# Kernel tuning notes

Measured on AMD Instinct MI355X. Metric: run time of the kernel, lower is better.

The kernel has to match this reference:

```python
import jax, jax.numpy as jnp
import numpy as np
from jax import lax


def setup_inputs() -> dict:
    key = jax.random.key(0)
    k1, k2 = jax.random.split(key)
    x = jax.random.normal(k1, (16, 224, 224, 256), dtype=jnp.float32)
    # Conv2D(1, 7): kernel HWIO [7,7,2,1], glorot-ish scale
    conv_w = jax.random.normal(k2, (7, 7, 2, 1), dtype=jnp.float32) * 0.1
    conv_b = jnp.zeros((1,), dtype=jnp.float32)
    return {"x": x, "conv_w": conv_w, "conv_b": conv_b}


def reference(x, conv_w, conv_b):
    # channel-wise stats: [B,H,W,1] each
    max_pool = jnp.max(x, axis=-1, keepdims=True)
    avg_pool = jnp.mean(x, axis=-1, keepdims=True)
    concat = jnp.concatenate([max_pool, avg_pool], axis=-1)  # [B,H,W,2]
    attn = lax.conv_general_dilated(
        concat, conv_w,
        window_strides=(1, 1), padding='SAME',
        dimension_numbers=('NHWC', 'HWIO', 'NHWC'))
    attn = jax.nn.sigmoid(attn + conv_b)  # [B,H,W,1]
    return x * attn
```

## Files before the change

kernel.cpp:

```cpp
#include <hip/hip_runtime.h>
#include <math.h>

#define B_ 16
#define H_ 224
#define W_ 224
#define C_ 256
#define IMGPIX (H_*W_)
#define NBLK 2048
#define NWAVE (NBLK*4)
#define NGRP  (NBLK*16)

typedef float f32x4 __attribute__((ext_vector_type(4)));

__device__ __forceinline__ void mul_role(const float* __restrict__ x,
                                         const float* __restrict__ cw,
                                         const float* __restrict__ cb,
                                         float* __restrict__ out,
                                         const float2* __restrict__ pooled,
                                         int mb0, int t) {
    const int lane = t & 63;
    float wm = 0.0f, wa = 0.0f;
    if (lane < 49) { wm = cw[lane * 2]; wa = cw[lane * 2 + 1]; }
    const float bias = cb[0];
    const int kh = lane / 7 - 3;
    const int kw = lane % 7 - 3;
    const int gw = blockIdx.x * 4 + (t >> 6);

    for (int q = gw; q < 2 * IMGPIX; q += NWAVE) {
        const int img = q / IMGPIX;
        const int px  = q - img * IMGPIX;
        const int b   = mb0 + img;
        const float*  xb    = x   + (size_t)b * IMGPIX * C_;
        float*        ob    = out + (size_t)b * IMGPIX * C_;
        const float2* pbase = pooled + (size_t)b * IMGPIX;

        const int h = px / W_, w = px % W_;
        float acc = 0.0f;
        if (lane < 49) {
            const int hh = h + kh, ww = w + kw;
            if (hh >= 0 && hh < H_ && ww >= 0 && ww < W_) {
                const float2 pv = pbase[hh * W_ + ww];
                acc = fmaf(pv.x, wm, pv.y * wa);
            }
        }
        #pragma unroll
        for (int off = 1; off < 64; off <<= 1) acc += __shfl_xor(acc, off);
        const float attn = 1.0f / (1.0f + expf(-(acc + bias)));

        f32x4 v = ((const f32x4*)(xb + (size_t)px * C_))[lane];
        v.x *= attn; v.y *= attn; v.z *= attn; v.w *= attn;
        __builtin_nontemporal_store(v, &((f32x4*)ob)[(size_t)px * 64 + lane]);
    }
}

__device__ __forceinline__ void pool_role(const float* __restrict__ x,
                                          float2* __restrict__ pooled,
                                          int pb0, int t) {
    const int gg  = blockIdx.x * 16 + (t >> 4);
    const int sub = t & 15;

    for (int q = gg; q < 2 * IMGPIX; q += NGRP) {
        const int img = q / IMGPIX;
        const int px  = q - img * IMGPIX;
        const int b   = pb0 + img;
        const float* xb  = x + (size_t)b * IMGPIX * C_;
        float2*      pot = pooled + (size_t)b * IMGPIX;

        const f32x4* p4 = (const f32x4*)(xb + (size_t)px * C_);
        float m = -INFINITY, s = 0.0f;
        #pragma unroll
        for (int j = 0; j < 4; ++j) {
            f32x4 v = p4[j * 16 + sub];
            m = fmaxf(m, fmaxf(fmaxf(v.x, v.y), fmaxf(v.z, v.w)));
            s += (v.x + v.y) + (v.z + v.w);
        }
        #pragma unroll
        for (int off = 1; off < 16; off <<= 1) {
            m = fmaxf(m, __shfl_xor(m, off));
            s += __shfl_xor(s, off);
        }
        if (sub == 0) pot[px] = make_float2(m, s * (1.0f / 256.0f));
    }
}

__global__ __launch_bounds__(256) void step_kernel(const float* __restrict__ x,
                                                   const float* __restrict__ cw,
                                                   const float* __restrict__ cb,
                                                   float* __restrict__ out,
                                                   float2* __restrict__ pooled,
                                                   int mb0, int pb0) {
    const int t = threadIdx.x;
    if (blockIdx.x & 1) {
        if (mb0 >= 0) mul_role(x, cw, cb, out, pooled, mb0, t);
        if (pb0 >= 0) pool_role(x, pooled, pb0, t);
    } else {
        if (pb0 >= 0) pool_role(x, pooled, pb0, t);
        if (mb0 >= 0) mul_role(x, cw, cb, out, pooled, mb0, t);
    }
}

extern "C" void kernel_launch(void* const* d_in, const int* in_sizes, int n_in,
                              void* d_out, int out_size, void* d_ws, size_t ws_size,
                              hipStream_t stream) {
    const float* x  = (const float*)d_in[0];
    const float* cw = (const float*)d_in[1];
    const float* cb = (const float*)d_in[2];
    float* out      = (float*)d_out;
    float2* pooled  = (float2*)d_ws;

    for (int d = 0; d <= 8; ++d) {
        const int mb0 = (d >= 1) ? 2 * (d - 1) : -1;
        const int pb0 = (d < 8) ? 2 * d : -1;
        step_kernel<<<NBLK, 256, 0, stream>>>(x, cw, cb, out, pooled, mb0, pb0);
    }
}
```

Baseline: 412.6 us.

## Split conv/sigmoid into separate pipeline stage writing a per-pixel attention map

The 7x7 conv and sigmoid move out of the multiply pass into their own attn_role, which writes a per-pixel attention map to workspace. The launch sequence becomes a three-stage software pipeline (pool, attn, mul) over 10 launches, with block roles rotated by blockIdx%3. The multiply pass now reads only x and one attention scalar per pixel, dropping the 49-tap gather and shuffle reduction from the bandwidth-bound loop. In exchange it adds one extra launch, an extra workspace array and its traffic, and unbalanced role ordering across blocks.

```diff
diff --git a/kernel.cpp b/kernel.cpp
--- a/kernel.cpp
+++ b/kernel.cpp
@@ -12,61 +12,16 @@
 
 typedef float f32x4 __attribute__((ext_vector_type(4)));
 
-__device__ __forceinline__ void mul_role(const float* __restrict__ x,
-                                         const float* __restrict__ cw,
-                                         const float* __restrict__ cb,
-                                         float* __restrict__ out,
-                                         const float2* __restrict__ pooled,
-                                         int mb0, int t) {
-    const int lane = t & 63;
-    float wm = 0.0f, wa = 0.0f;
-    if (lane < 49) { wm = cw[lane * 2]; wa = cw[lane * 2 + 1]; }
-    const float bias = cb[0];
-    const int kh = lane / 7 - 3;
-    const int kw = lane % 7 - 3;
-    const int gw = blockIdx.x * 4 + (t >> 6);
-
-    for (int q = gw; q < 2 * IMGPIX; q += NWAVE) {
-        const int img = q / IMGPIX;
-        const int px  = q - img * IMGPIX;
-        const int b   = mb0 + img;
-        const float*  xb    = x   + (size_t)b * IMGPIX * C_;
-        float*        ob    = out + (size_t)b * IMGPIX * C_;
-        const float2* pbase = pooled + (size_t)b * IMGPIX;
-
-        const int h = px / W_, w = px % W_;
-        float acc = 0.0f;
-        if (lane < 49) {
-            const int hh = h + kh, ww = w + kw;
-            if (hh >= 0 && hh < H_ && ww >= 0 && ww < W_) {
-                const float2 pv = pbase[hh * W_ + ww];
-                acc = fmaf(pv.x, wm, pv.y * wa);
-            }
-        }
-        #pragma unroll
-        for (int off = 1; off < 64; off <<= 1) acc += __shfl_xor(acc, off);
-        const float attn = 1.0f / (1.0f + expf(-(acc + bias)));
-
-        f32x4 v = ((const f32x4*)(xb + (size_t)px * C_))[lane];
-        v.x *= attn; v.y *= attn; v.z *= attn; v.w *= attn;
-        __builtin_nontemporal_store(v, &((f32x4*)ob)[(size_t)px * 64 + lane]);
-    }
-}
-
 __device__ __forceinline__ void pool_role(const float* __restrict__ x,
                                           float2* __restrict__ pooled,
                                           int pb0, int t) {
     const int gg  = blockIdx.x * 16 + (t >> 4);
     const int sub = t & 15;
-
     for (int q = gg; q < 2 * IMGPIX; q += NGRP) {
         const int img = q / IMGPIX;
         const int px  = q - img * IMGPIX;
         const int b   = pb0 + img;
-        const float* xb  = x + (size_t)b * IMGPIX * C_;
-        float2*      pot = pooled + (size_t)b * IMGPIX;
-
-        const f32x4* p4 = (const f32x4*)(xb + (size_t)px * C_);
+        const f32x4* p4 = (const f32x4*)(x + ((size_t)b * IMGPIX + px) * C_);
         float m = -INFINITY, s = 0.0f;
         #pragma unroll
         for (int j = 0; j < 4; ++j) {
@@ -79,7 +34,58 @@
             m = fmaxf(m, __shfl_xor(m, off));
             s += __shfl_xor(s, off);
         }
-        if (sub == 0) pot[px] = make_float2(m, s * (1.0f / 256.0f));
+        if (sub == 0) pooled[(size_t)b * IMGPIX + px] = make_float2(m, s * (1.0f / 256.0f));
+    }
+}
+
+__device__ __forceinline__ void attn_role(const float* __restrict__ cw,
+                                          const float* __restrict__ cb,
+                                          const float2* __restrict__ pooled,
+                                          float* __restrict__ attnmap,
+                                          int ab0, int t) {
+    const int lane = t & 63;
+    float wm = 0.0f, wa = 0.0f;
+    if (lane < 49) { wm = cw[lane * 2]; wa = cw[lane * 2 + 1]; }
+    const float bias = cb[0];
+    const int kh = lane / 7 - 3;
+    const int kw = lane % 7 - 3;
+    const int gw = blockIdx.x * 4 + (t >> 6);
+
+    for (int q = gw; q < 2 * IMGPIX; q += NWAVE) {
+        const int img = q / IMGPIX;
+        const int px  = q - img * IMGPIX;
+        const int b   = ab0 + img;
+        const float2* pbase = pooled + (size_t)b * IMGPIX;
+        const int h = px / W_, w = px % W_;
+        float acc = 0.0f;
+        if (lane < 49) {
+            const int hh = h + kh, ww = w + kw;
+            if (hh >= 0 && hh < H_ && ww >= 0 && ww < W_) {
+                const float2 pv = pbase[hh * W_ + ww];
+                acc = fmaf(pv.x, wm, pv.y * wa);
+            }
+        }
+        #pragma unroll
+        for (int off = 1; off < 64; off <<= 1) acc += __shfl_xor(acc, off);
+        if (lane == 0)
+            attnmap[(size_t)b * IMGPIX + px] = 1.0f / (1.0f + expf(-(acc + bias)));
+    }
+}
+
+__device__ __forceinline__ void mul_role(const float* __restrict__ x,
+                                         const float* __restrict__ attnmap,
+                                         float* __restrict__ out,
+                                         int mb0, int t) {
+    const int lane = t & 63;
+    const int gw = blockIdx.x * 4 + (t >> 6);
+    for (int q = gw; q < 2 * IMGPIX; q += NWAVE) {
+        const int img = q / IMGPIX;
+        const int px  = q - img * IMGPIX;
+        const size_t gp = (size_t)(mb0 + img) * IMGPIX + px;
+        const float a = attnmap[gp];
+        f32x4 v = ((const f32x4*)(x + gp * C_))[lane];
+        v.x *= a; v.y *= a; v.z *= a; v.w *= a;
+        __builtin_nontemporal_store(v, &((f32x4*)(out + gp * C_))[lane]);
     }
 }
 
@@ -88,14 +94,25 @@
                                                    const float* __restrict__ cb,
                                                    float* __restrict__ out,
                                                    float2* __restrict__ pooled,
-                                                   int mb0, int pb0) {
+                                                   float* __restrict__ attnmap,
+                                                   int mb0, int ab0, int pb0) {
     const int t = threadIdx.x;
-    if (blockIdx.x & 1) {
-        if (mb0 >= 0) mul_role(x, cw, cb, out, pooled, mb0, t);
+    switch (blockIdx.x % 3) {
+    case 0:
+        if (mb0 >= 0) mul_role(x, attnmap, out, mb0, t);
         if (pb0 >= 0) pool_role(x, pooled, pb0, t);
-    } else {
+        if (ab0 >= 0) attn_role(cw, cb, pooled, attnmap, ab0, t);
+        break;
+    case 1:
         if (pb0 >= 0) pool_role(x, pooled, pb0, t);
-        if (mb0 >= 0) mul_role(x, cw, cb, out, pooled, mb0, t);
+        if (mb0 >= 0) mul_role(x, attnmap, out, mb0, t);
+        if (ab0 >= 0) attn_role(cw, cb, pooled, attnmap, ab0, t);
+        break;
+    default:
+        if (ab0 >= 0) attn_role(cw, cb, pooled, attnmap, ab0, t);
+        if (mb0 >= 0) mul_role(x, attnmap, out, mb0, t);
+        if (pb0 >= 0) pool_role(x, pooled, pb0, t);
+        break;
     }
 }
 
@@ -107,10 +124,13 @@
     const float* cb = (const float*)d_in[2];
     float* out      = (float*)d_out;
     float2* pooled  = (float2*)d_ws;
+    float* attnmap  = (float*)((char*)d_ws + (size_t)B_ * IMGPIX * sizeof(float2));
 
-    for (int d = 0; d <= 8; ++d) {
-        const int mb0 = (d >= 1) ? 2 * (d - 1) : -1;
-        const int pb0 = (d < 8) ? 2 * d : -1;
-        step_kernel<<<NBLK, 256, 0, stream>>>(x, cw, cb, out, pooled, mb0, pb0);
+    for (int d = 0; d <= 9; ++d) {
+        const int pb0 = (d <= 7) ? 2 * d : -1;
+        const int ab0 = (d >= 1 && d <= 8) ? 2 * (d - 1) : -1;
+        const int mb0 = (d >= 2) ? 2 * (d - 2) : -1;
+        step_kernel<<<NBLK, 256, 0, stream>>>(x, cw, cb, out, pooled, attnmap,
+                                              mb0, ab0, pb0);
     }
 }
```

Result: slower. 486.5 us (+17.9%).
